# Performance work log

Measured on AMD Instinct MI355X. Metric: run time of the kernel, lower is better.

The kernel has to match this reference:

```python
import jax, jax.numpy as jnp
import numpy as np

V, E, H = 32000, 512, 1024
B, T = 32, 64

def setup_inputs() -> dict:
    key = jax.random.key(0)
    ks = jax.random.split(key, 8)
    return {
        "x": jax.random.randint(ks[0], (B, T), 0, V, dtype=jnp.int32),
        "state_h": jax.random.normal(ks[1], (B, H), dtype=jnp.float32),
        "state_c": jax.random.normal(ks[2], (B, H), dtype=jnp.float32),
        "emb_table": jax.random.normal(ks[3], (V, E), dtype=jnp.float32) * 0.02,
        "W": jax.random.normal(ks[4], (E, 4 * H), dtype=jnp.float32) * (1.0 / np.sqrt(E)),
        "U": jax.random.normal(ks[5], (H, 4 * H), dtype=jnp.float32) * (1.0 / np.sqrt(H)),
        "b": jnp.zeros((4 * H,), dtype=jnp.float32),
        "dense_W": jax.random.normal(ks[6], (H, V), dtype=jnp.float32) * (1.0 / np.sqrt(H)),
        "dense_b": jnp.zeros((V,), dtype=jnp.float32),
    }

def _lstm(emb, h0, c0, W, U, b):
    # Precompute input projections for all timesteps: [B,T,4H]
    xW = jnp.einsum('bte,eg->btg', emb, W) + b
    def step(carry, xw_t):
        h, c = carry
        z = xw_t + h @ U  # [B,4H]
        i, f, g, o = jnp.split(z, 4, axis=-1)  # Keras gate order i,f,c,o
        i = jax.nn.sigmoid(i)
        f = jax.nn.sigmoid(f)
        g = jnp.tanh(g)
        o = jax.nn.sigmoid(o)
        c = f * c + i * g
        h = o * jnp.tanh(c)
        return (h, c), h
    (h, c), hs = jax.lax.scan(step, (h0, c0), xW.transpose(1, 0, 2))
    return hs.transpose(1, 0, 2), h, c  # [B,T,H], [B,H], [B,H]

def reference(x, state_h, state_c, emb_table, W, U, b, dense_W, dense_b):
    emb = emb_table[x]  # [B,T,E]
    seq, h, c = _lstm(emb, state_h, state_c, W, U, b)
    logits = jnp.einsum('bth,hv->btv', seq, dense_W) + dense_b  # [B,T,V]
    return logits, h, c
```

## Files before the change

kernel.cpp:

```cpp
#include <hip/hip_runtime.h>

typedef unsigned short u16;
typedef __bf16 bf16x8 __attribute__((ext_vector_type(8)));
typedef float f32x4 __attribute__((ext_vector_type(4)));
typedef u16 u16x8 __attribute__((ext_vector_type(8)));
typedef u16 u16x4 __attribute__((ext_vector_type(4)));

#define T_STEPS 64
#define BATCH 32
#define HDIM 1024
#define EDIM 512
#define VDIM 32000
#define GDIM 4096

__device__ __forceinline__ u16 f2b(float v) {
  unsigned x = __float_as_uint(v);
  return (u16)((x + 0x7fffu + ((x >> 16) & 1u)) >> 16);
}

__device__ __forceinline__ void gload16(const void* g, void* l) {
  __builtin_amdgcn_global_load_lds(
      (const __attribute__((address_space(1))) void*)g,
      (__attribute__((address_space(3))) void*)l, 16, 0, 0);
}

__device__ __forceinline__ f32x4 mfma16(bf16x8 a, bf16x8 b, f32x4 c) {
  return __builtin_amdgcn_mfma_f32_16x16x32_bf16(a, b, c, 0, 0, 0);
}


__global__ __launch_bounds__(256) void gather_emb_k(
    const int* __restrict__ x, const float* __restrict__ emb,
    u16* __restrict__ A) {
  int bt = blockIdx.x;
  int tok = x[bt];
  const float4* src = (const float4*)(emb + (size_t)tok * EDIM);
  u16x4* dst = (u16x4*)(A + (size_t)bt * EDIM);
  if (threadIdx.x < 128) {
    float4 v = src[threadIdx.x];
    u16x4 o = {f2b(v.x), f2b(v.y), f2b(v.z), f2b(v.w)};
    dst[threadIdx.x] = o;
  }
}

__global__ __launch_bounds__(256) void transpose_cvt_k(
    const float* __restrict__ in, u16* __restrict__ out, int K, int N) {
  __shared__ u16 tile[64][80];
  int n0 = blockIdx.x * 64, k0 = blockIdx.y * 64;
  int tid = threadIdx.x;
  int r0 = tid >> 4;
  int c4 = (tid & 15) * 4;
#pragma unroll
  for (int rr = 0; rr < 4; ++rr) {
    int r = rr * 16 + r0;
    float4 v = *reinterpret_cast<const float4*>(
        &in[(size_t)(k0 + r) * N + n0 + c4]);
    tile[c4 + 0][r] = f2b(v.x);
    tile[c4 + 1][r] = f2b(v.y);
    tile[c4 + 2][r] = f2b(v.z);
    tile[c4 + 3][r] = f2b(v.w);
  }
  __syncthreads();
  int wr2 = tid >> 3, c8 = (tid & 7) * 8;
#pragma unroll
  for (int rr = 0; rr < 2; ++rr) {
    int r = rr * 32 + wr2;
    *reinterpret_cast<u16x8*>(&out[(size_t)(n0 + r) * K + k0 + c8]) =
        *reinterpret_cast<const u16x8*>(&tile[r][c8]);
  }
}

__global__ __launch_bounds__(256) void transpose_cvt_permU_k(
    const float* __restrict__ in, u16* __restrict__ out) {
  const int K = HDIM, N = GDIM;
  __shared__ u16 tile[64][80];
  int n0 = blockIdx.x * 64, k0 = blockIdx.y * 64;
  int tid = threadIdx.x;
  int r0 = tid >> 4;
  int c4 = (tid & 15) * 4;
#pragma unroll
  for (int rr = 0; rr < 4; ++rr) {
    int r = rr * 16 + r0;
    float4 v = *reinterpret_cast<const float4*>(
        &in[(size_t)(k0 + r) * N + n0 + c4]);
    tile[c4 + 0][r] = f2b(v.x);
    tile[c4 + 1][r] = f2b(v.y);
    tile[c4 + 2][r] = f2b(v.z);
    tile[c4 + 3][r] = f2b(v.w);
  }
  __syncthreads();
  int wr2 = tid >> 3, c8 = (tid & 7) * 8;
#pragma unroll
  for (int rr = 0; rr < 2; ++rr) {
    int r = rr * 32 + wr2;
    int n = n0 + r;
    int g = n >> 10, c = n & 1023;
    int pn = ((c >> 2) << 4) + (g << 2) + (c & 3);
    *reinterpret_cast<u16x8*>(&out[(size_t)pn * K + k0 + c8]) =
        *reinterpret_cast<const u16x8*>(&tile[r][c8]);
  }
}

__global__ __launch_bounds__(256) void init_state_k(
    const float* __restrict__ h0, const float* __restrict__ c0,
    u16* __restrict__ h0b, float* __restrict__ c_ws) {
  int i = blockIdx.x * 256 + threadIdx.x;
  h0b[i] = f2b(h0[i]);
  c_ws[i] = c0[i];
}


__global__ __launch_bounds__(256) void gemm_bf16_k(
    const u16* __restrict__ A, const u16* __restrict__ BT,
    const float* __restrict__ bias, float* __restrict__ C,
    int M, int N, int K) {
  __shared__ u16 As[128 * 64];
  __shared__ u16 Bs[128 * 64];
  const int tid = threadIdx.x;
  const int w = tid >> 6, lane = tid & 63;
  const int lo16 = lane & 15, hi4 = lane >> 4;
  const int nmb = gridDim.y;
  const int bid = blockIdx.y * gridDim.x + blockIdx.x;
  const int m0 = (bid % nmb) * 128, n0 = (bid / nmb) * 128;
  const int wr = w >> 1, wc = w & 1;
  f32x4 acc[4][4] = {};

  const int srow = lane >> 3;
  const int scol = (lane & 7) * 8;

  for (int k0 = 0; k0 < K; k0 += 64) {
    __syncthreads();
#pragma unroll
    for (int r = 0; r < 4; ++r) {
      int blkrow = (r * 4 + w) * 8 + srow;
      gload16(A + (size_t)(m0 + blkrow) * K + k0 + scol,
              As + (r * 4 + w) * 512);
      gload16(BT + (size_t)(n0 + blkrow) * K + k0 + scol,
              Bs + (r * 4 + w) * 512);
    }
    __syncthreads();

    bf16x8 af[4][2], bfr[4][2];
#pragma unroll
    for (int mi = 0; mi < 4; ++mi)
#pragma unroll
      for (int kk = 0; kk < 2; ++kk)
        af[mi][kk] = *reinterpret_cast<const bf16x8*>(
            As + (wr * 64 + mi * 16 + lo16) * 64 + kk * 32 + hi4 * 8);
#pragma unroll
    for (int nj = 0; nj < 4; ++nj)
#pragma unroll
      for (int kk = 0; kk < 2; ++kk)
        bfr[nj][kk] = *reinterpret_cast<const bf16x8*>(
            Bs + (wc * 64 + nj * 16 + lo16) * 64 + kk * 32 + hi4 * 8);
#pragma unroll
    for (int mi = 0; mi < 4; ++mi)
#pragma unroll
      for (int nj = 0; nj < 4; ++nj)
#pragma unroll
        for (int kk = 0; kk < 2; ++kk)
          acc[mi][nj] = mfma16(af[mi][kk], bfr[nj][kk], acc[mi][nj]);
  }

  const int row0 = m0 + wr * 64, col0 = n0 + wc * 64;
#pragma unroll
  for (int mi = 0; mi < 4; ++mi) {
#pragma unroll
    for (int nj = 0; nj < 4; ++nj) {
      int col = col0 + nj * 16 + lo16;
      float bv = bias ? bias[col] : 0.f;
#pragma unroll
      for (int j = 0; j < 4; ++j) {
        int row = row0 + mi * 16 + hi4 * 4 + j;
        C[(size_t)row * N + col] = acc[mi][nj][j] + bv;
      }
    }
  }
}


#define STG_A(dst, h, kb)                                              \
  do {                                                                 \
    gload16(Abytes + offA[h][0] + (kb), (dst) + (h) * 16384 + w * 1024); \
    gload16(Abytes + offA[h][1] + (kb),                                \
            (dst) + (h) * 16384 + 8192 + w * 1024);                    \
  } while (0)
#define STG_B(dst, h, kb)                                              \
  do {                                                                 \
    gload16(Bbytes + offB[h][0] + (kb),                                \
            (dst) + 32768 + (h) * 16384 + w * 1024);                   \
    gload16(Bbytes + offB[h][1] + (kb),                                \
            (dst) + 32768 + (h) * 16384 + 8192 + w * 1024);            \
  } while (0)
#define VMW4 asm volatile("s_waitcnt vmcnt(4)" ::: "memory")
#define VMW0 asm volatile("s_waitcnt vmcnt(0)" ::: "memory")

#define PHASE(cur, mih, njh, STG, WAIT)                                   \
  do {                                                                    \
    bf16x8 af[4][2], bfr[2][2];                                           \
    _Pragma("unroll") for (int u = 0; u < 4; ++u) {                       \
      af[u][0] = *reinterpret_cast<const bf16x8*>((cur) +                 \
                                                  aoff[(mih)*4 + u][0]);  \
      af[u][1] = *reinterpret_cast<const bf16x8*>((cur) +                 \
                                                  aoff[(mih)*4 + u][1]);  \
    }                                                                     \
    _Pragma("unroll") for (int v = 0; v < 2; ++v) {                       \
      bfr[v][0] = *reinterpret_cast<const bf16x8*>((cur) +                \
                                                   boff[(njh)*2 + v][0]); \
      bfr[v][1] = *reinterpret_cast<const bf16x8*>((cur) +                \
                                                   boff[(njh)*2 + v][1]); \
    }                                                                     \
    STG;                                                                  \
    __builtin_amdgcn_s_barrier();                                         \
    asm volatile("s_waitcnt lgkmcnt(0)" ::: "memory");                    \
    __builtin_amdgcn_s_setprio(1);                                        \
    _Pragma("unroll") for (int u = 0; u < 4; ++u)                         \
        _Pragma("unroll") for (int v = 0; v < 2; ++v) {                   \
      acc[(mih)*4 + u][(njh)*2 + v] =                                     \
          mfma16(af[u][0], bfr[v][0], acc[(mih)*4 + u][(njh)*2 + v]);     \
      acc[(mih)*4 + u][(njh)*2 + v] =                                     \
          mfma16(af[u][1], bfr[v][1], acc[(mih)*4 + u][(njh)*2 + v]);     \
    }                                                                     \
    __builtin_amdgcn_s_setprio(0);                                        \
    WAIT;                                                                 \
    __builtin_amdgcn_s_barrier();                                         \
  } while (0)

__global__ __launch_bounds__(512, 2) void gemm256_k(
    const u16* __restrict__ A,
    const u16* __restrict__ BT,
    const float* __restrict__ bias,
    float* __restrict__ C,
    int M, int N, int K) {
  __shared__ __attribute__((aligned(1024))) char smem[131072];
  const int tid = threadIdx.x;
  const int w = tid >> 6, lane = tid & 63;
  const int lo16 = lane & 15, hi4 = lane >> 4;
  const int wr = w >> 2, wc = w & 3;

  const int cpx = gridDim.x >> 3;
  const int bid = blockIdx.x;
  const int swz = (bid & 7) * cpx + (bid >> 3);
  const int nmb = M >> 8;
  const int m0 = (swz % nmb) << 8, n0 = (swz / nmb) << 8;

  const char* Abytes = (const char*)A;
  const char* Bbytes = (const char*)BT;
  const int K2 = K * 2;

  int offA[2][2], offB[2][2];
#pragma unroll
  for (int h = 0; h < 2; ++h)
#pragma unroll
    for (int i = 0; i < 2; ++i) {
      int o = h * 16384 + (i * 512 + tid) * 16;
      int s = o >> 10, q = o & 1023;
      int qp = q ^ (((q >> 9) & 1) << 5);
      int row = ((s >> 1) << 4) + (qp >> 6);
      int colb = ((s & 1) << 6) + (qp & 63);
      offA[h][i] = (m0 + row) * K2 + colb;
      offB[h][i] = (n0 + row) * K2 + colb;
    }

  int aoff[8][2], boff[4][2];
#pragma unroll
  for (int mi = 0; mi < 8; ++mi)
#pragma unroll
    for (int kk = 0; kk < 2; ++kk) {
      int r = (mi >> 2) * 128 + wr * 64 + (mi & 3) * 16 + lo16;
      int q = (r & 15) * 64 + hi4 * 16;
      int qs = q ^ (((q >> 9) & 1) << 5);
      aoff[mi][kk] = (((r >> 4) << 1) + kk) * 1024 + qs;
    }
#pragma unroll
  for (int nj = 0; nj < 4; ++nj)
#pragma unroll
    for (int kk = 0; kk < 2; ++kk) {
      int r = (nj >> 1) * 128 + wc * 32 + (nj & 1) * 16 + lo16;
      int q = (r & 15) * 64 + hi4 * 16;
      int qs = q ^ (((q >> 9) & 1) << 5);
      boff[nj][kk] = 32768 + (((r >> 4) << 1) + kk) * 1024 + qs;
    }

  f32x4 acc[8][4] = {};
  char* const bd = smem;
  char* const bo = smem + 65536;

  STG_A(bd, 0, 0);
  STG_B(bd, 0, 0);
  STG_A(bd, 1, 0);
  STG_B(bd, 1, 0);
  STG_A(bo, 0, 128);
  STG_B(bo, 0, 128);
  VMW4;
  __builtin_amdgcn_s_barrier();

  const int NITER = K >> 7;
  for (int it = 0; it < NITER - 1; ++it) {
    const int k1 = (it * 128 + 64) * 2;
    const int k2 = (it * 128 + 128) * 2;
    const int k3 = (it * 128 + 192) * 2;
    PHASE(bd, 0, 0, STG_A(bo, 1, k1), ((void)0));
    PHASE(bd, 0, 1, STG_B(bo, 1, k1), ((void)0));
    PHASE(bd, 1, 0, STG_A(bd, 0, k2), ((void)0));
    PHASE(bd, 1, 1, STG_B(bd, 0, k2), VMW4);
    PHASE(bo, 0, 0, STG_A(bd, 1, k2), ((void)0));
    PHASE(bo, 0, 1, STG_B(bd, 1, k2), ((void)0));
    PHASE(bo, 1, 0, STG_A(bo, 0, k3), ((void)0));
    PHASE(bo, 1, 1, STG_B(bo, 0, k3), VMW4);
  }
  {
    const int k1 = ((NITER - 1) * 128 + 64) * 2;
    PHASE(bd, 0, 0, STG_A(bo, 1, k1), ((void)0));
    PHASE(bd, 0, 1, STG_B(bo, 1, k1), ((void)0));
    PHASE(bd, 1, 0, ((void)0), ((void)0));
    PHASE(bd, 1, 1, ((void)0), VMW0);
    PHASE(bo, 0, 0, ((void)0), ((void)0));
    PHASE(bo, 0, 1, ((void)0), ((void)0));
    PHASE(bo, 1, 0, ((void)0), ((void)0));
    PHASE(bo, 1, 1, ((void)0), ((void)0));
  }

#pragma unroll
  for (int mi = 0; mi < 8; ++mi) {
    int row = m0 + (mi >> 2) * 128 + wr * 64 + (mi & 3) * 16 + hi4 * 4;
#pragma unroll
    for (int nj = 0; nj < 4; ++nj) {
      int col = n0 + (nj >> 1) * 128 + wc * 32 + (nj & 1) * 16 + lo16;
      float bv = bias ? bias[col] : 0.f;
#pragma unroll
      for (int j = 0; j < 4; ++j)
        C[(size_t)(row + j) * N + col] = acc[mi][nj][j] + bv;
    }
  }
}


__global__ __launch_bounds__(512) void lstm_step3_k(
    const float* __restrict__ xW,
    const u16* __restrict__ h_src,
    int h_stride,
    const u16* __restrict__ UT2,
    float* __restrict__ c_ws,
    u16* __restrict__ seq,
    float* __restrict__ out_hc,
    int t) {
  __shared__ float Zs[2][4][16][17];
  const int tid = threadIdx.x;
  const int w = tid >> 6, lane = tid & 63;
  const int lo16 = lane & 15, hi4 = lane >> 4;
  const int bt = w >> 2, wq = w & 3;
  const int zt = blockIdx.x;

  const int b_e = tid >> 2, jg = tid & 3;
  float xw0 = 0.f, xw1 = 0.f, xw2 = 0.f, xw3 = 0.f;
  if (tid < 128) {
    const float* xrow =
        xW + (size_t)(b_e * T_STEPS + t) * GDIM + zt * 4 + jg;
    xw0 = xrow[0];
    xw1 = xrow[1024];
    xw2 = xrow[2048];
    xw3 = xrow[3072];
  }

  const u16* arow = h_src + (size_t)(bt * 16 + lo16) * h_stride;
  const u16* brow = UT2 + (size_t)(zt * 16 + lo16) * HDIM;

  f32x4 acc = {};
#pragma unroll
  for (int kc = 0; kc < 8; ++kc) {
    int k = wq * 256 + kc * 32 + hi4 * 8;
    bf16x8 a = *reinterpret_cast<const bf16x8*>(arow + k);
    bf16x8 b = *reinterpret_cast<const bf16x8*>(brow + k);
    acc = mfma16(a, b, acc);
  }
#pragma unroll
  for (int j = 0; j < 4; ++j) Zs[bt][wq][hi4 * 4 + j][lo16] = acc[j];
  __syncthreads();

  if (tid < 128) {
    int hcol = zt * 4 + jg;
    float z[4] = {xw0, xw1, xw2, xw3};
#pragma unroll
    for (int g = 0; g < 4; ++g)
#pragma unroll
      for (int ww = 0; ww < 4; ++ww)
        z[g] += Zs[b_e >> 4][ww][b_e & 15][g * 4 + jg];
    size_t cidx = (size_t)b_e * HDIM + hcol;
    float c_old = c_ws[cidx];
    float ig = 1.f / (1.f + __expf(-z[0]));
    float fg = 1.f / (1.f + __expf(-z[1]));
    float gg = tanhf(z[2]);
    float og = 1.f / (1.f + __expf(-z[3]));
    float cn = fg * c_old + ig * gg;
    float hn = og * tanhf(cn);
    c_ws[cidx] = cn;
    seq[(size_t)(b_e * T_STEPS + t) * HDIM + hcol] = f2b(hn);
    if (out_hc) {
      out_hc[cidx] = hn;
      out_hc[BATCH * HDIM + cidx] = cn;
    }
  }
}


extern "C" void kernel_launch(void* const* d_in, const int* in_sizes, int n_in,
                              void* d_out, int out_size, void* d_ws,
                              size_t ws_size, hipStream_t stream) {
  const int* x = (const int*)d_in[0];
  const float* state_h = (const float*)d_in[1];
  const float* state_c = (const float*)d_in[2];
  const float* emb = (const float*)d_in[3];
  const float* W = (const float*)d_in[4];
  const float* U = (const float*)d_in[5];
  const float* bvec = (const float*)d_in[6];
  const float* dW = (const float*)d_in[7];
  const float* db = (const float*)d_in[8];
  float* out = (float*)d_out;
  char* ws = (char*)d_ws;

  size_t off = 0;
  auto alloc = [&](size_t bytes) {
    void* p = ws + off;
    off += (bytes + 255) & ~(size_t)255;
    return p;
  };
  u16* A_emb = (u16*)alloc(2048ull * EDIM * 2);
  u16* WbT   = (u16*)alloc((size_t)GDIM * EDIM * 2);
  u16* UT2   = (u16*)alloc((size_t)GDIM * HDIM * 2);
  u16* DbT   = (u16*)alloc((size_t)VDIM * HDIM * 2);
  float* xW  = (float*)alloc(2048ull * GDIM * 4);
  u16* seq   = (u16*)alloc(2048ull * HDIM * 2);
  u16* h0b   = (u16*)alloc((size_t)BATCH * HDIM * 2);
  float* c_ws = (float*)alloc((size_t)BATCH * HDIM * 4);
  if (off > ws_size) return;

  gather_emb_k<<<2048, 256, 0, stream>>>(x, emb, A_emb);
  transpose_cvt_k<<<dim3(GDIM / 64, EDIM / 64), 256, 0, stream>>>(W, WbT, EDIM, GDIM);
  transpose_cvt_permU_k<<<dim3(GDIM / 64, HDIM / 64), 256, 0, stream>>>(U, UT2);
  transpose_cvt_k<<<dim3(VDIM / 64, HDIM / 64), 256, 0, stream>>>(dW, DbT, HDIM, VDIM);
  init_state_k<<<128, 256, 0, stream>>>(state_h, state_c, h0b, c_ws);

  gemm_bf16_k<<<dim3(GDIM / 128, 2048 / 128), 256, 0, stream>>>(
      A_emb, WbT, bvec, xW, 2048, GDIM, EDIM);

  for (int t = 0; t < T_STEPS; ++t) {
    const u16* h_src = (t == 0) ? h0b : (seq + (size_t)(t - 1) * HDIM);
    int h_stride = (t == 0) ? HDIM : T_STEPS * HDIM;
    float* outhc = (t == T_STEPS - 1) ? (out + 65536000ull) : nullptr;
    lstm_step3_k<<<256, 512, 0, stream>>>(xW, h_src, h_stride, UT2, c_ws, seq,
                                          outhc, t);
  }

  gemm256_k<<<dim3((2048 / 256) * (VDIM / 256)), 512, 0, stream>>>(
      seq, DbT, db, out, 2048, VDIM, HDIM);
}
```

Baseline: 716.7 us.

## Split LSTM step across batch halves, ping-pong compact h buffer, reorder GEMM staging

The recurrent step kernel now launches 512 blocks of 256 threads, each block handling one 16-row batch half instead of both halves per block. The new hidden state is also written to a contiguous ping-pong buffer, so the next step reads h with a dense stride instead of the strided seq layout. In the big output GEMM, the global-to-LDS prefetch is issued before the LDS fragment reads rather than after, giving it more time to overlap. The trade-off is that each step reads U twice as often across blocks and writes h an extra time.

```diff
diff --git a/kernel.cpp b/kernel.cpp
--- a/kernel.cpp
+++ b/kernel.cpp
@@ -197,6 +197,7 @@
 
 #define PHASE(cur, mih, njh, STG, WAIT)                                   \
   do {                                                                    \
+    STG;                                                                  \
     bf16x8 af[4][2], bfr[2][2];                                           \
     _Pragma("unroll") for (int u = 0; u < 4; ++u) {                       \
       af[u][0] = *reinterpret_cast<const bf16x8*>((cur) +                 \
@@ -210,7 +211,6 @@
       bfr[v][1] = *reinterpret_cast<const bf16x8*>((cur) +                \
                                                    boff[(njh)*2 + v][1]); \
     }                                                                     \
-    STG;                                                                  \
     __builtin_amdgcn_s_barrier();                                         \
     asm volatile("s_waitcnt lgkmcnt(0)" ::: "memory");                    \
     __builtin_amdgcn_s_setprio(1);                                        \
@@ -336,57 +336,57 @@
 }
 
 
-__global__ __launch_bounds__(512) void lstm_step3_k(
+__global__ __launch_bounds__(256) void lstm_step2_k(
     const float* __restrict__ xW,
     const u16* __restrict__ h_src,
-    int h_stride,
     const u16* __restrict__ UT2,
     float* __restrict__ c_ws,
+    u16* __restrict__ h_dst,
     u16* __restrict__ seq,
     float* __restrict__ out_hc,
     int t) {
-  __shared__ float Zs[2][4][16][17];
+  __shared__ float Zs[4][16][17];
   const int tid = threadIdx.x;
   const int w = tid >> 6, lane = tid & 63;
   const int lo16 = lane & 15, hi4 = lane >> 4;
-  const int bt = w >> 2, wq = w & 3;
-  const int zt = blockIdx.x;
-
-  const int b_e = tid >> 2, jg = tid & 3;
+  const int zt = blockIdx.x >> 1;
+  const int bt = blockIdx.x & 1;
+
+  const int bb = tid >> 2, jg = tid & 3;
   float xw0 = 0.f, xw1 = 0.f, xw2 = 0.f, xw3 = 0.f;
-  if (tid < 128) {
+  if (tid < 64) {
     const float* xrow =
-        xW + (size_t)(b_e * T_STEPS + t) * GDIM + zt * 4 + jg;
+        xW + (size_t)((bt * 16 + bb) * T_STEPS + t) * GDIM + zt * 4 + jg;
     xw0 = xrow[0];
     xw1 = xrow[1024];
     xw2 = xrow[2048];
     xw3 = xrow[3072];
   }
 
-  const u16* arow = h_src + (size_t)(bt * 16 + lo16) * h_stride;
+  const u16* arow = h_src + (size_t)(bt * 16 + lo16) * HDIM;
   const u16* brow = UT2 + (size_t)(zt * 16 + lo16) * HDIM;
 
   f32x4 acc = {};
 #pragma unroll
   for (int kc = 0; kc < 8; ++kc) {
-    int k = wq * 256 + kc * 32 + hi4 * 8;
+    int k = w * 256 + kc * 32 + hi4 * 8;
     bf16x8 a = *reinterpret_cast<const bf16x8*>(arow + k);
     bf16x8 b = *reinterpret_cast<const bf16x8*>(brow + k);
     acc = mfma16(a, b, acc);
   }
 #pragma unroll
-  for (int j = 0; j < 4; ++j) Zs[bt][wq][hi4 * 4 + j][lo16] = acc[j];
+  for (int j = 0; j < 4; ++j) Zs[w][hi4 * 4 + j][lo16] = acc[j];
   __syncthreads();
 
-  if (tid < 128) {
+  if (tid < 64) {
+    int b = bt * 16 + bb;
     int hcol = zt * 4 + jg;
     float z[4] = {xw0, xw1, xw2, xw3};
 #pragma unroll
     for (int g = 0; g < 4; ++g)
 #pragma unroll
-      for (int ww = 0; ww < 4; ++ww)
-        z[g] += Zs[b_e >> 4][ww][b_e & 15][g * 4 + jg];
-    size_t cidx = (size_t)b_e * HDIM + hcol;
+      for (int ww = 0; ww < 4; ++ww) z[g] += Zs[ww][bb][g * 4 + jg];
+    size_t cidx = (size_t)b * HDIM + hcol;
     float c_old = c_ws[cidx];
     float ig = 1.f / (1.f + __expf(-z[0]));
     float fg = 1.f / (1.f + __expf(-z[1]));
@@ -395,7 +395,9 @@
     float cn = fg * c_old + ig * gg;
     float hn = og * tanhf(cn);
     c_ws[cidx] = cn;
-    seq[(size_t)(b_e * T_STEPS + t) * HDIM + hcol] = f2b(hn);
+    u16 hb = f2b(hn);
+    h_dst[cidx] = hb;
+    seq[(size_t)(b * T_STEPS + t) * HDIM + hcol] = hb;
     if (out_hc) {
       out_hc[cidx] = hn;
       out_hc[BATCH * HDIM + cidx] = cn;
@@ -432,6 +434,7 @@
   float* xW  = (float*)alloc(2048ull * GDIM * 4);
   u16* seq   = (u16*)alloc(2048ull * HDIM * 2);
   u16* h0b   = (u16*)alloc((size_t)BATCH * HDIM * 2);
+  u16* hbuf  = (u16*)alloc(2ull * BATCH * HDIM * 2);
   float* c_ws = (float*)alloc((size_t)BATCH * HDIM * 4);
   if (off > ws_size) return;
 
@@ -445,10 +448,10 @@
       A_emb, WbT, bvec, xW, 2048, GDIM, EDIM);
 
   for (int t = 0; t < T_STEPS; ++t) {
-    const u16* h_src = (t == 0) ? h0b : (seq + (size_t)(t - 1) * HDIM);
-    int h_stride = (t == 0) ? HDIM : T_STEPS * HDIM;
+    const u16* h_src = (t == 0) ? h0b : (hbuf + (size_t)(t & 1) * (BATCH * HDIM));
+    u16* h_dst = hbuf + (size_t)((t + 1) & 1) * (BATCH * HDIM);
     float* outhc = (t == T_STEPS - 1) ? (out + 65536000ull) : nullptr;
-    lstm_step3_k<<<256, 512, 0, stream>>>(xW, h_src, h_stride, UT2, c_ws, seq,
+    lstm_step2_k<<<512, 256, 0, stream>>>(xW, h_src, UT2, c_ws, h_dst, seq,
                                           outhc, t);
   }
 
```

Result: faster. 667.1 us (-6.9%).
